# Kernel optimization log

Hardware: AMD Instinct MI355X
Metric: run time of the kernel (lower is better)

The kernel has to match this reference:

```python
import jax, jax.numpy as jnp
import numpy as np

B, C_IN, C_OUT, N, K = 8, 64, 128, 2048, 16
EPS = 1e-5  # torch BatchNorm2d default


def setup_inputs() -> dict:
    key = jax.random.key(0)
    ks = jax.random.split(key, 2)
    x = jax.random.normal(ks[0], (B, C_IN, N, 1), dtype=jnp.float32)
    # Conv2d(2*C_IN, C_OUT, 1) kaiming_normal weight, zero bias; 1x1 kernel -> [C_OUT, 2*C_IN]
    W = jax.random.normal(ks[1], (C_OUT, 2 * C_IN), dtype=jnp.float32) * np.float32(np.sqrt(2.0 / (2 * C_IN)))
    b = jnp.zeros((C_OUT,), jnp.float32)
    gamma = jnp.ones((C_OUT,), jnp.float32)   # BN weight filled with 1
    beta = jnp.zeros((C_OUT,), jnp.float32)   # BN bias zeroed
    return {"x": x, "W": W, "b": b, "gamma": gamma, "beta": beta, "k": K}


def reference(x, W, b, gamma, beta, k):
    # x: [B, C, N, 1]
    xs = x[..., 0]                              # [B, C, N]
    feats = jnp.transpose(xs, (0, 2, 1))        # [B, N, C]
    # knn: pairwise_distance = -||xi||^2 + 2 xi.xj - ||xj||^2 (negative sq dist)
    sq = jnp.sum(xs * xs, axis=1)               # [B, N]
    gram = jnp.einsum('bcn,bcm->bnm', xs, xs)   # [B, N, N]
    pd = 2.0 * gram - sq[:, :, None] - sq[:, None, :]
    idx = jax.lax.top_k(pd, k)[1]               # [B, N, k] neighbor indices
    # gather: x_j = neighbor features, x_i = center features broadcast over k
    x_j = jnp.take_along_axis(feats[:, None, :, :], idx[:, :, :, None], axis=2)  # [B, N, k, C]
    x_i = feats[:, :, None, :]                  # [B, N, 1, C]
    e = jnp.concatenate([jnp.broadcast_to(x_i, x_j.shape), x_j - x_i], axis=-1)  # [B, N, k, 2C]
    # 1x1 conv (matmul over channels) + ReLU
    h = jax.nn.relu(jnp.einsum('bnkc,oc->bnko', e, W) + b)  # [B, N, k, O]
    # BatchNorm2d in training mode: batch stats over (B, N, k), biased variance
    mean = jnp.mean(h, axis=(0, 1, 2))
    var = jnp.mean(jnp.square(h - mean), axis=(0, 1, 2))
    h = (h - mean) * jax.lax.rsqrt(var + EPS) * gamma + beta
    # max over neighbors, back to [B, O, N, 1]
    out = jnp.max(h, axis=2)                    # [B, N, O]
    return jnp.transpose(out, (0, 2, 1))[..., None]
```

## Files before the change

kernel.cpp:

```cpp
#include <hip/hip_runtime.h>
#include <math.h>

#define BB 8
#define CIN 64
#define CO 128
#define NPT 2048
#define KK 16
#define EPSV 1e-5f
#define LOSCALE 2048.0f

typedef unsigned int u32;
typedef unsigned long long u64;
typedef _Float16 f16x8 __attribute__((ext_vector_type(8)));
typedef float f32x4 __attribute__((ext_vector_type(4)));

__global__ __launch_bounds__(256) void k_prep_pv(
    const float* __restrict__ x, const float* __restrict__ W,
    const float* __restrict__ bias, float* __restrict__ sq,
    _Float16* __restrict__ xh, _Float16* __restrict__ xl,
    float* __restrict__ p, float* __restrict__ v) {
  __shared__ float tile[64][65];
  __shared__ float tileT[64][68];
  __shared__ float psum[4][64];
  int bid = blockIdx.x;
  int b = bid >> 5;
  int n0 = (bid & 31) << 6;
  int tid = threadIdx.x;
  int q = tid >> 6, lo = tid & 63;
#pragma unroll
  for (int i = 0; i < 16; ++i) {
    int c = i * 4 + q;
    tile[c][lo] = x[((size_t)(b * CIN + c)) * NPT + n0 + lo];
  }
  __syncthreads();
  float ps = 0.f;
#pragma unroll
  for (int i = 0; i < 16; ++i) {
    float t = tile[q * 16 + i][lo];
    ps += t * t;
  }
  psum[q][lo] = ps;
#pragma unroll
  for (int i = 0; i < 16; ++i) {
    int ni = i * 4 + q;
    float val = tile[lo][ni];
    tileT[ni][lo] = val;
    size_t o = ((size_t)(b * NPT + n0 + ni)) * CIN + lo;
    _Float16 h = (_Float16)val;
    xh[o] = h;
    xl[o] = (_Float16)((val - (float)h) * LOSCALE);
  }
  __syncthreads();
  if (q == 0) {
    sq[(size_t)b * NPT + n0 + lo] = psum[0][lo] + psum[1][lo] + psum[2][lo] + psum[3][lo];
  }
  int o = tid & 127, hh = tid >> 7;
  const float4* W1 = (const float4*)&W[o * 2 * CIN];
  const float4* W2 = (const float4*)&W[o * 2 * CIN + CIN];
  float bo = bias[o];
#pragma unroll 2
  for (int t = 0; t < 32; ++t) {
    int node = t * 2 + hh;
    float a1 = 0.f, a2 = 0.f;
#pragma unroll
    for (int c4 = 0; c4 < 16; ++c4) {
      float4 xv = *(const float4*)&tileT[node][c4 * 4];
      float4 w1 = W1[c4];
      float4 w2 = W2[c4];
      a1 += xv.x * w1.x + xv.y * w1.y + xv.z * w1.z + xv.w * w1.w;
      a2 += xv.x * w2.x + xv.y * w2.y + xv.z * w2.z + xv.w * w2.w;
    }
    size_t gn = ((size_t)(b * NPT + n0 + node)) * CO + o;
    p[gn] = a1 - a2 + bo;
    v[gn] = a2;
  }
}

__global__ __launch_bounds__(1024) void k_dist_topk(
    const _Float16* __restrict__ xh, const _Float16* __restrict__ xl,
    const float* __restrict__ sq, int* __restrict__ idxout) {
  __shared__ uint4 tiles[16][2][256];
  __shared__ float submax[16][64];
  __shared__ float2 cand[16][96];
  __shared__ int cnt[16];
  __shared__ float tauf[16];

  int bid = (blockIdx.x & 7) * 128 + (blockIdx.x >> 3);
  int b = bid >> 7;
  int rt = (bid & 127) << 4;
  int tid = threadIdx.x;
  int w = tid >> 6, lane = tid & 63;
  int lr = lane & 15, lg = lane >> 4;
  const _Float16* xhb = xh + (size_t)b * NPT * CIN;
  const _Float16* xlb = xl + (size_t)b * NPT * CIN;
  const float* sqb = sq + (size_t)b * NPT;

  if (tid < 16) cnt[tid] = 0;

  const size_t arow = (size_t)(rt + lr) * CIN + lg * 8;
  f16x8 ah0 = *(const f16x8*)(xhb + arow);
  f16x8 ah1 = *(const f16x8*)(xhb + arow + 32);
  f16x8 al0 = *(const f16x8*)(xlb + arow);
  f16x8 al1 = *(const f16x8*)(xlb + arow + 32);
  float4 sqr = *(const float4*)(sqb + rt + lg * 4);
  float sqrv[4] = {sqr.x, sqr.y, sqr.z, sqr.w};
  float csqs[8];
#pragma unroll
  for (int t = 0; t < 8; ++t) csqs[t] = sqb[(w * 8 + t) * 16 + lr];

  const char* xhB = (const char*)xhb;
  const char* xlB = (const char*)xlb;
  const int su = (lane ^ ((lane >> 3) & 7)) * 16;

#define ISSUE_TILE(T)                                                          \
  {                                                                            \
    const int tb_ = (w * 8 + (T)) * 2048;                                      \
    uint4* buf_ = &tiles[w][(T) & 1][0];                                       \
    __builtin_amdgcn_global_load_lds((const uint4*)(xhB + tb_ + su),           \
                                     buf_, 16, 0, 0);                          \
    __builtin_amdgcn_global_load_lds((const uint4*)(xhB + tb_ + 1024 + su),    \
                                     buf_ + 64, 16, 0, 0);                     \
    __builtin_amdgcn_global_load_lds((const uint4*)(xlB + tb_ + su),           \
                                     buf_ + 128, 16, 0, 0);                    \
    __builtin_amdgcn_global_load_lds((const uint4*)(xlB + tb_ + 1024 + su),    \
                                     buf_ + 192, 16, 0, 0);                    \
  }

  ISSUE_TILE(0)
  ISSUE_TILE(1)

  const int uh0 = lr * 8 + (lg ^ (lr & 7));
  const int uh1 = lr * 8 + ((lg + 4) ^ (lr & 7));
  float vals[32];

#pragma unroll
  for (int t = 0; t < 8; ++t) {
    if (t < 7) { asm volatile("s_waitcnt vmcnt(4)" ::: "memory"); }
    else       { asm volatile("s_waitcnt vmcnt(0)" ::: "memory"); }
    __builtin_amdgcn_sched_barrier(0);
    const uint4* bufr = &tiles[w][t & 1][0];
    f16x8 bh0 = *(const f16x8*)(bufr + uh0);
    f16x8 bh1 = *(const f16x8*)(bufr + uh1);
    f16x8 bl0 = *(const f16x8*)(bufr + 128 + uh0);
    f16x8 bl1 = *(const f16x8*)(bufr + 128 + uh1);
    f32x4 acc0 = {0.f, 0.f, 0.f, 0.f};
    f32x4 acc1 = {0.f, 0.f, 0.f, 0.f};
    acc1 = __builtin_amdgcn_mfma_f32_16x16x32_f16(ah0, bl0, acc1, 0, 0, 0);
    acc1 = __builtin_amdgcn_mfma_f32_16x16x32_f16(al0, bh0, acc1, 0, 0, 0);
    acc1 = __builtin_amdgcn_mfma_f32_16x16x32_f16(ah1, bl1, acc1, 0, 0, 0);
    acc1 = __builtin_amdgcn_mfma_f32_16x16x32_f16(al1, bh1, acc1, 0, 0, 0);
    acc0 = __builtin_amdgcn_mfma_f32_16x16x32_f16(ah0, bh0, acc0, 0, 0, 0);
    acc0 = __builtin_amdgcn_mfma_f32_16x16x32_f16(ah1, bh1, acc0, 0, 0, 0);
    const float k2 = 2.0f / LOSCALE;
#pragma unroll
    for (int q = 0; q < 4; ++q) {
      vals[t * 4 + q] = fmaf(acc1[q], k2, 2.f * acc0[q]) - (sqrv[q] + csqs[t]);
    }
    asm volatile("s_waitcnt lgkmcnt(0)" ::: "memory");
    __builtin_amdgcn_sched_barrier(0);
    if (t == 0) ISSUE_TILE(2)
    if (t == 1) ISSUE_TILE(3)
    if (t == 2) ISSUE_TILE(4)
    if (t == 3) ISSUE_TILE(5)
    if (t == 4) ISSUE_TILE(6)
    if (t == 5) ISSUE_TILE(7)
  }
#undef ISSUE_TILE

  float rmax[4];
#pragma unroll
  for (int q = 0; q < 4; ++q) {
    float m = vals[q];
#pragma unroll
    for (int t = 1; t < 8; ++t) m = fmaxf(m, vals[t * 4 + q]);
    m = fmaxf(m, __shfl_xor(m, 1, 64));
    m = fmaxf(m, __shfl_xor(m, 2, 64));
    rmax[q] = m;
  }
  if ((lr & 3) == 0) {
    int pool = w * 4 + (lr >> 2);
#pragma unroll
    for (int q = 0; q < 4; ++q) submax[lg * 4 + q][pool] = rmax[q];
  }
  __syncthreads();

  {
    u32 ou = __float_as_uint(submax[w][lane]);
    ou = (ou & 0x80000000u) ? ~ou : (ou | 0x80000000u);
    u32 lo = 0u;
#pragma unroll
    for (int s2 = 31; s2 >= 16; --s2) {
      u32 cd = lo | (1u << s2);
      u64 bal = __ballot(ou >= cd);
      if (__popcll(bal) >= KK) lo = cd;
    }
    u32 tb = (lo & 0x80000000u) ? (lo ^ 0x80000000u) : ~lo;
    if (lane == 0) tauf[w] = __uint_as_float(tb);
  }
  __syncthreads();

  {
    float tq[4];
#pragma unroll
    for (int q = 0; q < 4; ++q) tq[q] = tauf[lg * 4 + q];
#pragma unroll
    for (int t = 0; t < 8; ++t) {
#pragma unroll
      for (int q = 0; q < 4; ++q) {
        float vv = vals[t * 4 + q];
        if (vv >= tq[q]) {
          int r = lg * 4 + q;
          int pos = atomicAdd(&cnt[r], 1);
          if (pos < 96) cand[r][pos] = make_float2(vv, __int_as_float((w * 8 + t) * 16 + lr));
        }
      }
    }
  }
  __syncthreads();

  int total = cnt[w];
  if (total > 96) total = 96;
  const float NINF = -__builtin_inff();
  float cv = NINF;
  int ci = 0x7FFFFFFF;
  int n1 = total < 64 ? total : 64;
  if (lane < n1) {
    float2 pr = cand[w][lane];
    cv = pr.x; ci = __float_as_int(pr.y);
  }

#define PSORT(KMAX)                                                        \
  _Pragma("unroll") for (int k = 2; k <= (KMAX); k <<= 1) {                \
    _Pragma("unroll") for (int j = k >> 1; j > 0; j >>= 1) {               \
      float pv = __shfl_xor(cv, j, 64);                                    \
      int pi = __shfl_xor(ci, j, 64);                                      \
      bool up = (lane & k) != 0;                                           \
      bool lw = (lane & j) == 0;                                           \
      bool gt = (cv > pv) || (cv == pv && ci < pi);                        \
      bool keep = (lw != up) ? gt : !gt;                                   \
      cv = keep ? cv : pv;                                                 \
      ci = keep ? ci : pi;                                                 \
    }                                                                      \
  }

  if (total > 32) {
    PSORT(64)
    if (total > 64) {
      if (lane >= 16) {
        int src2 = 48 + lane;
        if (src2 < total) {
          float2 pr = cand[w][src2];
          cv = pr.x; ci = __float_as_int(pr.y);
        } else { cv = NINF; ci = 0x7FFFFFFF; }
      }
      PSORT(64)
    }
  } else {
    PSORT(32)
  }
#undef PSORT

  if (lane < KK) idxout[((size_t)(b * NPT + rt + w)) * KK + lane] = ci;
}

__global__ __launch_bounds__(256) void k_stats(
    const float* __restrict__ p, const float* __restrict__ v,
    const int* __restrict__ idx, float* __restrict__ psums,
    float* __restrict__ psqs, float* __restrict__ mxb) {
  __shared__ float rs[8][CO];
  __shared__ float rq[8][CO];
  int bid = (blockIdx.x & 7) * 128 + (blockIdx.x >> 3);
  int b = bid >> 7;
  int n0 = (bid & 127) << 4;
  int tid = threadIdx.x;
  int o4 = tid & 31, ns = tid >> 5;
  const float* vb = v + (size_t)b * NPT * CO;
  float4 s = {0.f, 0.f, 0.f, 0.f};
  float4 qq = {0.f, 0.f, 0.f, 0.f};
#pragma unroll 1
  for (int g = 0; g < 2; ++g) {
    int gn = b * NPT + n0 + g * 8 + ns;
    size_t po = (size_t)gn * CO + o4 * 4;
    float4 p4 = *(const float4*)(p + po);
    const int* id = idx + (size_t)gn * KK;
    int4 j0 = *(const int4*)(id);
    int4 j1 = *(const int4*)(id + 4);
    int4 j2 = *(const int4*)(id + 8);
    int4 j3 = *(const int4*)(id + 12);
    int jj[16] = {j0.x, j0.y, j0.z, j0.w, j1.x, j1.y, j1.z, j1.w,
                  j2.x, j2.y, j2.z, j2.w, j3.x, j3.y, j3.z, j3.w};
    float4 mx4 = {-1e30f, -1e30f, -1e30f, -1e30f};
#pragma unroll
    for (int k = 0; k < KK; ++k) {
      float4 v4 = *(const float4*)(vb + (size_t)jj[k] * CO + o4 * 4);
      float h0 = fmaxf(p4.x + v4.x, 0.f);
      float h1 = fmaxf(p4.y + v4.y, 0.f);
      float h2 = fmaxf(p4.z + v4.z, 0.f);
      float h3 = fmaxf(p4.w + v4.w, 0.f);
      s.x += h0; s.y += h1; s.z += h2; s.w += h3;
      qq.x += h0 * h0; qq.y += h1 * h1; qq.z += h2 * h2; qq.w += h3 * h3;
      mx4.x = fmaxf(mx4.x, h0); mx4.y = fmaxf(mx4.y, h1);
      mx4.z = fmaxf(mx4.z, h2); mx4.w = fmaxf(mx4.w, h3);
    }
    *(float4*)(mxb + po) = mx4;
  }
  rs[ns][o4 * 4 + 0] = s.x;  rs[ns][o4 * 4 + 1] = s.y;
  rs[ns][o4 * 4 + 2] = s.z;  rs[ns][o4 * 4 + 3] = s.w;
  rq[ns][o4 * 4 + 0] = qq.x; rq[ns][o4 * 4 + 1] = qq.y;
  rq[ns][o4 * 4 + 2] = qq.z; rq[ns][o4 * 4 + 3] = qq.w;
  __syncthreads();
  if (tid < CO) {
    float ts = 0.f, tq = 0.f;
#pragma unroll
    for (int i = 0; i < 8; ++i) { ts += rs[i][tid]; tq += rq[i][tid]; }
    psums[(size_t)bid * CO + tid] = ts;
    psqs[(size_t)bid * CO + tid] = tq;
  }
}

__global__ __launch_bounds__(64) void k_final(
    const float* __restrict__ psums, const float* __restrict__ psqs,
    const float* __restrict__ gamma, const float* __restrict__ beta,
    float* __restrict__ scale, float* __restrict__ shift) {
  int o = blockIdx.x;
  int t = threadIdx.x;
  float s = 0.f, q = 0.f;
  for (int i = t; i < BB * (NPT / 16); i += 64) {
    s += psums[(size_t)i * CO + o];
    q += psqs[(size_t)i * CO + o];
  }
#pragma unroll
  for (int d = 32; d >= 1; d >>= 1) {
    s += __shfl_down(s, d, 64);
    q += __shfl_down(q, d, 64);
  }
  if (t == 0) {
    const float M = (float)(BB * NPT * KK);
    float mean = s / M;
    float var = q / M - mean * mean;
    float sc = gamma[o] * rsqrtf(var + EPSV);
    scale[o] = sc;
    shift[o] = beta[o] - mean * sc;
  }
}

__global__ __launch_bounds__(256) void k_out_fast(
    const float* __restrict__ mxb, const float* __restrict__ scale,
    const float* __restrict__ shift, float* __restrict__ out) {
  __shared__ float ob[32][132];
  int bid = blockIdx.x;
  int b = bid >> 6;
  int n0 = (bid & 63) << 5;
  int tid = threadIdx.x;
  int o4 = tid & 31, ns = tid >> 5;
  float4 sc = *(const float4*)(scale + o4 * 4);
  float4 sh = *(const float4*)(shift + o4 * 4);
#pragma unroll
  for (int g = 0; g < 4; ++g) {
    int node = g * 8 + ns;
    size_t po = (size_t)(b * NPT + n0 + node) * CO + o4 * 4;
    float4 mx = *(const float4*)(mxb + po);
    float4 r;
    r.x = mx.x * sc.x + sh.x;
    r.y = mx.y * sc.y + sh.y;
    r.z = mx.z * sc.z + sh.z;
    r.w = mx.w * sc.w + sh.w;
    *(float4*)&ob[node][o4 * 4] = r;
  }
  __syncthreads();
  int ni = tid & 31, oh = tid >> 5;
#pragma unroll
  for (int pass = 0; pass < 16; ++pass) {
    int o = pass * 8 + oh;
    out[((size_t)(b * CO + o)) * NPT + n0 + ni] = ob[ni][o];
  }
}

extern "C" void kernel_launch(void* const* d_in, const int* in_sizes, int n_in,
                              void* d_out, int out_size, void* d_ws, size_t ws_size,
                              hipStream_t stream) {
  const float* x = (const float*)d_in[0];
  const float* W = (const float*)d_in[1];
  const float* bias = (const float*)d_in[2];
  const float* gamma = (const float*)d_in[3];
  const float* beta = (const float*)d_in[4];
  float* out = (float*)d_out;

  char* ws = (char*)d_ws;
  size_t off = 0;
  auto alloc = [&](size_t bytes) {
    void* ptr = ws + off;
    off += (bytes + 255) & ~(size_t)255;
    return ptr;
  };
  float* ft = (float*)alloc(sizeof(float) * BB * NPT * CIN);
  _Float16* xh = (_Float16*)alloc(sizeof(_Float16) * BB * NPT * CIN);
  _Float16* xl = (_Float16*)alloc(sizeof(_Float16) * BB * NPT * CIN);
  float* mx = ft;
  float* sq = (float*)alloc(sizeof(float) * BB * NPT);
  float* p = (float*)alloc(sizeof(float) * BB * NPT * CO);
  float* v = (float*)alloc(sizeof(float) * BB * NPT * CO);
  int* idx = (int*)alloc(sizeof(int) * BB * NPT * KK);
  float* psums = (float*)alloc(sizeof(float) * BB * (NPT / 16) * CO);
  float* psqs = (float*)alloc(sizeof(float) * BB * (NPT / 16) * CO);
  float* scale = (float*)alloc(sizeof(float) * CO);
  float* shift = (float*)alloc(sizeof(float) * CO);
  (void)ws_size; (void)in_sizes; (void)n_in; (void)out_size;

  hipLaunchKernelGGL(k_prep_pv, dim3(BB * (NPT / 64)), dim3(256), 0, stream,
                     x, W, bias, sq, xh, xl, p, v);
  hipLaunchKernelGGL(k_dist_topk, dim3(BB * (NPT / 16)), dim3(1024), 0, stream, xh, xl, sq, idx);
  hipLaunchKernelGGL(k_stats, dim3(BB * (NPT / 16)), dim3(256), 0, stream, p, v, idx, psums, psqs, mx);
  hipLaunchKernelGGL(k_final, dim3(CO), dim3(64), 0, stream, psums, psqs, gamma, beta, scale, shift);
  hipLaunchKernelGGL(k_out_fast, dim3(BB * (NPT / 32)), dim3(256), 0, stream, mx, scale, shift, out);
}
```

Before: 110.2 us.

## Make distance-topk kernel persistent over four row tiles with prefetch overlap

The kNN distance/top-k kernel now launches 256 blocks, and each block loops over four consecutive 16-row tiles instead of handling one. The next tile's A-fragments and first B tiles are prefetched before the threshold selection and sort of the current tile, so those loads overlap that work. It also issues the next tile load before the MFMAs inside the inner loop. Per-block setup is amortised, at the cost of only 256 blocks of 1024 threads, which may underfill the GPU and leaves less parallelism to hide latency.

Result: slower. 158.8 us (+44.1%).

```diff
diff --git a/kernel.cpp b/kernel.cpp
--- a/kernel.cpp
+++ b/kernel.cpp
@@ -85,9 +85,8 @@
   __shared__ int cnt[16];
   __shared__ float tauf[16];
 
-  int bid = (blockIdx.x & 7) * 128 + (blockIdx.x >> 3);
-  int b = bid >> 7;
-  int rt = (bid & 127) << 4;
+  int b = blockIdx.x & 7;
+  int rg = blockIdx.x >> 3;
   int tid = threadIdx.x;
   int w = tid >> 6, lane = tid & 63;
   int lr = lane & 15, lg = lane >> 4;
@@ -97,13 +96,6 @@
 
   if (tid < 16) cnt[tid] = 0;
 
-  const size_t arow = (size_t)(rt + lr) * CIN + lg * 8;
-  f16x8 ah0 = *(const f16x8*)(xhb + arow);
-  f16x8 ah1 = *(const f16x8*)(xhb + arow + 32);
-  f16x8 al0 = *(const f16x8*)(xlb + arow);
-  f16x8 al1 = *(const f16x8*)(xlb + arow + 32);
-  float4 sqr = *(const float4*)(sqb + rt + lg * 4);
-  float sqrv[4] = {sqr.x, sqr.y, sqr.z, sqr.w};
   float csqs[8];
 #pragma unroll
   for (int t = 0; t < 8; ++t) csqs[t] = sqb[(w * 8 + t) * 16 + lr];
@@ -111,6 +103,8 @@
   const char* xhB = (const char*)xhb;
   const char* xlB = (const char*)xlb;
   const int su = (lane ^ ((lane >> 3) & 7)) * 16;
+  const int uh0 = lr * 8 + (lg ^ (lr & 7));
+  const int uh1 = lr * 8 + ((lg + 4) ^ (lr & 7));
 
 #define ISSUE_TILE(T)                                                          \
   {                                                                            \
@@ -126,108 +120,134 @@
                                      buf_ + 192, 16, 0, 0);                    \
   }
 
+  int rt = rg * 64;
+  size_t arow = (size_t)(rt + lr) * CIN + lg * 8;
+  f16x8 ah0 = *(const f16x8*)(xhb + arow);
+  f16x8 ah1 = *(const f16x8*)(xhb + arow + 32);
+  f16x8 al0 = *(const f16x8*)(xlb + arow);
+  f16x8 al1 = *(const f16x8*)(xlb + arow + 32);
+  float4 sqr = *(const float4*)(sqb + rt + lg * 4);
+  __builtin_amdgcn_sched_barrier(0);
   ISSUE_TILE(0)
   ISSUE_TILE(1)
-
-  const int uh0 = lr * 8 + (lg ^ (lr & 7));
-  const int uh1 = lr * 8 + ((lg + 4) ^ (lr & 7));
-  float vals[32];
-
-#pragma unroll
-  for (int t = 0; t < 8; ++t) {
-    if (t < 7) { asm volatile("s_waitcnt vmcnt(4)" ::: "memory"); }
-    else       { asm volatile("s_waitcnt vmcnt(0)" ::: "memory"); }
-    __builtin_amdgcn_sched_barrier(0);
-    const uint4* bufr = &tiles[w][t & 1][0];
-    f16x8 bh0 = *(const f16x8*)(bufr + uh0);
-    f16x8 bh1 = *(const f16x8*)(bufr + uh1);
-    f16x8 bl0 = *(const f16x8*)(bufr + 128 + uh0);
-    f16x8 bl1 = *(const f16x8*)(bufr + 128 + uh1);
-    f32x4 acc0 = {0.f, 0.f, 0.f, 0.f};
-    f32x4 acc1 = {0.f, 0.f, 0.f, 0.f};
-    acc1 = __builtin_amdgcn_mfma_f32_16x16x32_f16(ah0, bl0, acc1, 0, 0, 0);
-    acc1 = __builtin_amdgcn_mfma_f32_16x16x32_f16(al0, bh0, acc1, 0, 0, 0);
-    acc1 = __builtin_amdgcn_mfma_f32_16x16x32_f16(ah1, bl1, acc1, 0, 0, 0);
-    acc1 = __builtin_amdgcn_mfma_f32_16x16x32_f16(al1, bh1, acc1, 0, 0, 0);
-    acc0 = __builtin_amdgcn_mfma_f32_16x16x32_f16(ah0, bh0, acc0, 0, 0, 0);
-    acc0 = __builtin_amdgcn_mfma_f32_16x16x32_f16(ah1, bh1, acc0, 0, 0, 0);
-    const float k2 = 2.0f / LOSCALE;
-#pragma unroll
-    for (int q = 0; q < 4; ++q) {
-      vals[t * 4 + q] = fmaf(acc1[q], k2, 2.f * acc0[q]) - (sqrv[q] + csqs[t]);
-    }
-    asm volatile("s_waitcnt lgkmcnt(0)" ::: "memory");
-    __builtin_amdgcn_sched_barrier(0);
-    if (t == 0) ISSUE_TILE(2)
-    if (t == 1) ISSUE_TILE(3)
-    if (t == 2) ISSUE_TILE(4)
-    if (t == 3) ISSUE_TILE(5)
-    if (t == 4) ISSUE_TILE(6)
-    if (t == 5) ISSUE_TILE(7)
-  }
-#undef ISSUE_TILE
-
-  float rmax[4];
-#pragma unroll
-  for (int q = 0; q < 4; ++q) {
-    float m = vals[q];
-#pragma unroll
-    for (int t = 1; t < 8; ++t) m = fmaxf(m, vals[t * 4 + q]);
-    m = fmaxf(m, __shfl_xor(m, 1, 64));
-    m = fmaxf(m, __shfl_xor(m, 2, 64));
-    rmax[q] = m;
-  }
-  if ((lr & 3) == 0) {
-    int pool = w * 4 + (lr >> 2);
-#pragma unroll
-    for (int q = 0; q < 4; ++q) submax[lg * 4 + q][pool] = rmax[q];
-  }
-  __syncthreads();
-
-  {
-    u32 ou = __float_as_uint(submax[w][lane]);
-    ou = (ou & 0x80000000u) ? ~ou : (ou | 0x80000000u);
-    u32 lo = 0u;
-#pragma unroll
-    for (int s2 = 31; s2 >= 16; --s2) {
-      u32 cd = lo | (1u << s2);
-      u64 bal = __ballot(ou >= cd);
-      if (__popcll(bal) >= KK) lo = cd;
-    }
-    u32 tb = (lo & 0x80000000u) ? (lo ^ 0x80000000u) : ~lo;
-    if (lane == 0) tauf[w] = __uint_as_float(tb);
-  }
-  __syncthreads();
-
-  {
-    float tq[4];
-#pragma unroll
-    for (int q = 0; q < 4; ++q) tq[q] = tauf[lg * 4 + q];
+  __builtin_amdgcn_sched_barrier(0);
+
+#pragma unroll 1
+  for (int it = 0; it < 4; ++it) {
+    float sqrv[4] = {sqr.x, sqr.y, sqr.z, sqr.w};
+    float vals[32];
+
 #pragma unroll
     for (int t = 0; t < 8; ++t) {
+      if (t < 7) { asm volatile("s_waitcnt vmcnt(4)" ::: "memory"); }
+      else       { asm volatile("s_waitcnt vmcnt(0)" ::: "memory"); }
+      __builtin_amdgcn_sched_barrier(0);
+      const uint4* bufr = &tiles[w][t & 1][0];
+      f16x8 bh0 = *(const f16x8*)(bufr + uh0);
+      f16x8 bh1 = *(const f16x8*)(bufr + uh1);
+      f16x8 bl0 = *(const f16x8*)(bufr + 128 + uh0);
+      f16x8 bl1 = *(const f16x8*)(bufr + 128 + uh1);
+      asm volatile("s_waitcnt lgkmcnt(0)" ::: "memory");
+      __builtin_amdgcn_sched_barrier(0);
+      if (t == 0) ISSUE_TILE(2)
+      if (t == 1) ISSUE_TILE(3)
+      if (t == 2) ISSUE_TILE(4)
+      if (t == 3) ISSUE_TILE(5)
+      if (t == 4) ISSUE_TILE(6)
+      if (t == 5) ISSUE_TILE(7)
+      f32x4 acc0 = {0.f, 0.f, 0.f, 0.f};
+      f32x4 acc1 = {0.f, 0.f, 0.f, 0.f};
+      acc1 = __builtin_amdgcn_mfma_f32_16x16x32_f16(ah0, bl0, acc1, 0, 0, 0);
+      acc1 = __builtin_amdgcn_mfma_f32_16x16x32_f16(al0, bh0, acc1, 0, 0, 0);
+      acc1 = __builtin_amdgcn_mfma_f32_16x16x32_f16(ah1, bl1, acc1, 0, 0, 0);
+      acc1 = __builtin_amdgcn_mfma_f32_16x16x32_f16(al1, bh1, acc1, 0, 0, 0);
+      acc0 = __builtin_amdgcn_mfma_f32_16x16x32_f16(ah0, bh0, acc0, 0, 0, 0);
+      acc0 = __builtin_amdgcn_mfma_f32_16x16x32_f16(ah1, bh1, acc0, 0, 0, 0);
+      const float k2 = 2.0f / LOSCALE;
 #pragma unroll
       for (int q = 0; q < 4; ++q) {
-        float vv = vals[t * 4 + q];
-        if (vv >= tq[q]) {
-          int r = lg * 4 + q;
-          int pos = atomicAdd(&cnt[r], 1);
-          if (pos < 96) cand[r][pos] = make_float2(vv, __int_as_float((w * 8 + t) * 16 + lr));
+        vals[t * 4 + q] = fmaf(acc1[q], k2, 2.f * acc0[q]) - (sqrv[q] + csqs[t]);
+      }
+    }
+
+    if (it < 3) {
+      int nrt = rt + 16;
+      size_t arow2 = (size_t)(nrt + lr) * CIN + lg * 8;
+      ah0 = *(const f16x8*)(xhb + arow2);
+      ah1 = *(const f16x8*)(xhb + arow2 + 32);
+      al0 = *(const f16x8*)(xlb + arow2);
+      al1 = *(const f16x8*)(xlb + arow2 + 32);
+      sqr = *(const float4*)(sqb + nrt + lg * 4);
+      __builtin_amdgcn_sched_barrier(0);
+      ISSUE_TILE(0)
+      ISSUE_TILE(1)
+      __builtin_amdgcn_sched_barrier(0);
+    }
+
+    {
+      float rmax[4];
+#pragma unroll
+      for (int q = 0; q < 4; ++q) {
+        float m = vals[q];
+#pragma unroll
+        for (int t = 1; t < 8; ++t) m = fmaxf(m, vals[t * 4 + q]);
+        m = fmaxf(m, __shfl_xor(m, 1, 64));
+        m = fmaxf(m, __shfl_xor(m, 2, 64));
+        rmax[q] = m;
+      }
+      if ((lr & 3) == 0) {
+        int pool = w * 4 + (lr >> 2);
+#pragma unroll
+        for (int q = 0; q < 4; ++q) submax[lg * 4 + q][pool] = rmax[q];
+      }
+    }
+    __syncthreads();
+
+    {
+      u32 ou = __float_as_uint(submax[w][lane]);
+      ou = (ou & 0x80000000u) ? ~ou : (ou | 0x80000000u);
+      u32 lo = 0u;
+#pragma unroll
+      for (int s2 = 31; s2 >= 16; --s2) {
+        u32 cd = lo | (1u << s2);
+        u64 bal = __ballot(ou >= cd);
+        if (__popcll(bal) >= KK) lo = cd;
+      }
+      u32 tb = (lo & 0x80000000u) ? (lo ^ 0x80000000u) : ~lo;
+      if (lane == 0) tauf[w] = __uint_as_float(tb);
+    }
+    __syncthreads();
+
+    {
+      float tq[4];
+#pragma unroll
+      for (int q = 0; q < 4; ++q) tq[q] = tauf[lg * 4 + q];
+#pragma unroll
+      for (int t = 0; t < 8; ++t) {
+#pragma unroll
+        for (int q = 0; q < 4; ++q) {
+          float vv = vals[t * 4 + q];
+          if (vv >= tq[q]) {
+            int r = lg * 4 + q;
+            int pos = atomicAdd(&cnt[r], 1);
+            if (pos < 96) cand[r][pos] = make_float2(vv, __int_as_float((w * 8 + t) * 16 + lr));
+          }
         }
       }
     }
-  }
-  __syncthreads();
-
-  int total = cnt[w];
-  if (total > 96) total = 96;
-  const float NINF = -__builtin_inff();
-  float cv = NINF;
-  int ci = 0x7FFFFFFF;
-  int n1 = total < 64 ? total : 64;
-  if (lane < n1) {
-    float2 pr = cand[w][lane];
-    cv = pr.x; ci = __float_as_int(pr.y);
-  }
+    __syncthreads();
+
+    {
+      int total = cnt[w];
+      if (total > 96) total = 96;
+      const float NINF = -__builtin_inff();
+      float cv = NINF;
+      int ci = 0x7FFFFFFF;
+      int n1 = total < 64 ? total : 64;
+      if (lane < n1) {
+        float2 pr = cand[w][lane];
+        cv = pr.x; ci = __float_as_int(pr.y);
+      }
 
 #define PSORT(KMAX)                                                        \
   _Pragma("unroll") for (int k = 2; k <= (KMAX); k <<= 1) {                \
@@ -243,24 +263,31 @@
     }                                                                      \
   }
 
-  if (total > 32) {
-    PSORT(64)
-    if (total > 64) {
-      if (lane >= 16) {
-        int src2 = 48 + lane;
-        if (src2 < total) {
-          float2 pr = cand[w][src2];
-          cv = pr.x; ci = __float_as_int(pr.y);
-        } else { cv = NINF; ci = 0x7FFFFFFF; }
-      }
-      PSORT(64)
-    }
-  } else {
-    PSORT(32)
-  }
+      if (total > 32) {
+        PSORT(64)
+        if (total > 64) {
+          if (lane >= 16) {
+            int src2 = 48 + lane;
+            if (src2 < total) {
+              float2 pr = cand[w][src2];
+              cv = pr.x; ci = __float_as_int(pr.y);
+            } else { cv = NINF; ci = 0x7FFFFFFF; }
+          }
+          PSORT(64)
+        }
+      } else {
+        PSORT(32)
+      }
 #undef PSORT
 
-  if (lane < KK) idxout[((size_t)(b * NPT + rt + w)) * KK + lane] = ci;
+      if (lane < KK) idxout[((size_t)(b * NPT + rt + w)) * KK + lane] = ci;
+    }
+
+    __syncthreads();
+    if (tid < 16) cnt[tid] = 0;
+    rt += 16;
+  }
+#undef ISSUE_TILE
 }
 
 __global__ __launch_bounds__(256) void k_stats(
@@ -409,7 +436,7 @@
 
   hipLaunchKernelGGL(k_prep_pv, dim3(BB * (NPT / 64)), dim3(256), 0, stream,
                      x, W, bias, sq, xh, xl, p, v);
-  hipLaunchKernelGGL(k_dist_topk, dim3(BB * (NPT / 16)), dim3(1024), 0, stream, xh, xl, sq, idx);
+  hipLaunchKernelGGL(k_dist_topk, dim3(256), dim3(1024), 0, stream, xh, xl, sq, idx);
   hipLaunchKernelGGL(k_stats, dim3(BB * (NPT / 16)), dim3(256), 0, stream, p, v, idx, psums, psqs, mx);
   hipLaunchKernelGGL(k_final, dim3(CO), dim3(64), 0, stream, psums, psqs, gamma, beta, scale, shift);
   hipLaunchKernelGGL(k_out_fast, dim3(BB * (NPT / 32)), dim3(256), 0, stream, mx, scale, shift, out);
```
